# Performance work log

Hardware: AMD Instinct MI355X
Metric: run time of the kernel (lower is better)

The kernel has to match this reference:

```python
import jax, jax.numpy as jnp
import numpy as np

EPS = 1e-5
K = 20
LRELU = 0.2


def _bn(x, g, b, ch_axis):
    # inference BatchNorm with running_mean=0, running_var=1
    shape = [1] * x.ndim
    shape[ch_axis] = -1
    scale = (g / jnp.sqrt(1.0 + EPS)).reshape(shape)
    bias = b.reshape(shape)
    return x * scale + bias


def _lrelu(x):
    return jnp.where(x > 0, x, LRELU * x)


def _edge_conv(x, W, g, b):
    # x: (B, C, N) -> (B, C_out, N)
    B, C, N = x.shape
    xt = jnp.swapaxes(x, 1, 2)                      # (B, N, C)
    inner = -2.0 * jnp.einsum('bnc,bmc->bnm', xt, xt)
    xx = jnp.sum(xt * xt, axis=2)                   # (B, N)
    pdist = -xx[:, :, None] - inner - xx[:, None, :]  # negative sq dist (B,N,N)
    idx = jax.lax.top_k(pdist, K)[1]                # (B, N, K) nearest (incl. self)
    # gather neighbor features per batch: (C, N) indexed by (N, K) -> (C, N, K)
    neighbors = jax.vmap(lambda xf, id_: xf[:, id_])(x, idx)  # (B, C, N, K)
    center = jnp.broadcast_to(x[..., None], (B, C, N, K))
    edge = jnp.concatenate([center, neighbors - center], axis=1)  # (B, 2C, N, K)
    h = jnp.einsum('oc,bcnk->bonk', W, edge)        # 1x1 conv, no bias
    h = _lrelu(_bn(h, g, b, 1))
    return jnp.max(h, axis=-1)                      # (B, C_out, N)


def setup_inputs() -> dict:
    key = jax.random.key(0)
    ks = jax.random.split(key, 24)
    B, N = 4, 2048
    d = {}
    d['points'] = jax.random.normal(ks[0], (B, N, 3), dtype=jnp.float32)

    def w(k_, shape):
        return 0.1 * jax.random.normal(k_, shape, dtype=jnp.float32)

    def gam(k_, c):
        return 1.0 + 0.1 * jax.random.normal(k_, (c,), dtype=jnp.float32)

    def bet(k_, c):
        return 0.05 * jax.random.normal(k_, (c,), dtype=jnp.float32)

    # EdgeConv blocks: (out, 2*in)
    d['w1'], d['g1'], d['b1'] = w(ks[1], (64, 6)), gam(ks[2], 64), bet(ks[3], 64)
    d['w2'], d['g2'], d['b2'] = w(ks[4], (64, 128)), gam(ks[5], 64), bet(ks[6], 64)
    d['w3'], d['g3'], d['b3'] = w(ks[7], (128, 128)), gam(ks[8], 128), bet(ks[9], 128)
    d['w4'], d['g4'], d['b4'] = w(ks[10], (256, 256)), gam(ks[11], 256), bet(ks[12], 256)
    # conv5 1x1: 512 -> 1024
    d['w5'], d['g5'], d['b5'] = w(ks[13], (1024, 512)), gam(ks[14], 1024), bet(ks[15], 1024)
    # fc: 2048 -> 512 -> 256
    d['fw1'], d['fb1'] = w(ks[16], (512, 2048)), 0.05 * jax.random.normal(ks[17], (512,), dtype=jnp.float32)
    d['g6'], d['b6'] = gam(ks[18], 512), bet(ks[19], 512)
    d['fw2'], d['fb2'] = w(ks[20], (256, 512)), 0.05 * jax.random.normal(ks[21], (256,), dtype=jnp.float32)
    d['g7'], d['b7'] = gam(ks[22], 256), bet(ks[23], 256)
    return d


def reference(points, w1, g1, b1, w2, g2, b2, w3, g3, b3, w4, g4, b4,
              w5, g5, b5, fw1, fb1, g6, b6, fw2, fb2, g7, b7):
    x = jnp.swapaxes(points[:, :, :3], 1, 2)        # (B, 3, N)
    x1 = _edge_conv(x, w1, g1, b1)                  # (B, 64, N)
    x2 = _edge_conv(x1, w2, g2, b2)                 # (B, 64, N)
    x3 = _edge_conv(x2, w3, g3, b3)                 # (B, 128, N)
    x4 = _edge_conv(x3, w4, g4, b4)                 # (B, 256, N)
    h = jnp.concatenate([x1, x2, x3, x4], axis=1)   # (B, 512, N)
    h = _lrelu(_bn(jnp.einsum('oc,bcn->bon', w5, h), g5, b5, 1))  # (B, 1024, N)
    h_max = jnp.max(h, axis=-1)
    h_avg = jnp.mean(h, axis=-1)
    f = jnp.concatenate([h_max, h_avg], axis=1)     # (B, 2048)
    f = _lrelu(_bn(f @ fw1.T + fb1, g6, b6, 1))     # dropout = identity (eval)
    f = _bn(f @ fw2.T + fb2, g7, b7, 1)
    return f                                        # (B, 256)
```

## Files before the change

### kernel.cpp

```cpp
#include <hip/hip_runtime.h>
#include <hip/hip_bf16.h>
#include <float.h>

#define N_PTS 2048
#define B_SZ  4
#define KNN   20
#define LRELU_S 0.2f
#define FT    512
#define NPOOL 16

typedef __hip_bfloat16 bf16;
typedef __attribute__((ext_vector_type(8))) short short8v;
typedef __attribute__((ext_vector_type(4))) short short4v;
typedef __attribute__((ext_vector_type(4))) float floatx4;

__device__ __forceinline__ float b2f(const bf16 v) { return __bfloat162float(v); }
__device__ __forceinline__ float ldf(const float* p) { return *p; }
__device__ __forceinline__ float ldf(const bf16* p)  { return __bfloat162float(*p); }
__device__ __forceinline__ short8v ld8(const bf16* p) { return *(const short8v*)p; }
__device__ __forceinline__ unsigned umin(unsigned a, unsigned b) { return a < b ? a : b; }
__device__ __forceinline__ short bfbits(float f) {
    bf16 t = __float2bfloat16(f);
    return *reinterpret_cast<short*>(&t);
}

__device__ __forceinline__ void gload16(const void* g, void* l) {
    __builtin_amdgcn_global_load_lds(
        (const __attribute__((address_space(1))) void*)g,
        (__attribute__((address_space(3))) void*)l, 16, 0, 0);
}

__device__ __forceinline__ int sniff_body(const unsigned short* pts_hw) {
    int sane = 0;
    for (int j = 0; j < 64; ++j) {
        unsigned short v = pts_hw[2 * j];
        int e = (v >> 7) & 0xFF;
        if (e >= 100 && e <= 140) ++sane;
    }
    return (sane >= 32) ? 1 : 0;
}

__global__ void k_sniff(const unsigned short* __restrict__ pts_hw, int* __restrict__ flag) {
    if (threadIdx.x != 0 || blockIdx.x != 0) return;
    *flag = sniff_body(pts_hw);
}

struct WPack {
    const void* src[23];
    int off[24];
    int rows[23];
    int cols[23];
};

__device__ __forceinline__ void repack_body(const WPack& wp, int isb,
                                            float* __restrict__ dst, int i, int limit,
                                            int skip12) {
    if (i >= limit) return;
    int lo = 0, hi = 23;
    while (lo + 1 < hi) { int mid = (lo + hi) >> 1; if (i >= wp.off[mid]) lo = mid; else hi = mid; }
    if (skip12 && lo == 12) return;
    int j = i - wp.off[lo];
    float v = isb ? b2f(((const bf16*)wp.src[lo])[j]) : ((const float*)wp.src[lo])[j];
    int dj = j;
    int cols = wp.cols[lo];
    if (cols) dj = (j % cols) * wp.rows[lo] + (j / cols);
    dst[wp.off[lo] + dj] = v;
}

template<int C, int COUT>
__device__ __forceinline__ void wsplit_body(const void* __restrict__ W, int isb,
                                            bf16* __restrict__ dst, int i) {
    if (i >= COUT * C) return;
    int o = i / C, c = i % C;
    float w1 = isb ? b2f(((const bf16*)W)[(size_t)o * 2 * C + c])
                   : ((const float*)W)[(size_t)o * 2 * C + c];
    float w2 = isb ? b2f(((const bf16*)W)[(size_t)o * 2 * C + C + c])
                   : ((const float*)W)[(size_t)o * 2 * C + C + c];
    float wd = w1 - w2;
    bf16 h2 = __float2bfloat16(w2);
    bf16 hd = __float2bfloat16(wd);
    dst[i]                = h2;
    dst[COUT * C + i]     = __float2bfloat16(w2 - b2f(h2));
    dst[2 * COUT * C + i] = hd;
    dst[3 * COUT * C + i] = __float2bfloat16(wd - b2f(hd));
}

__device__ __forceinline__ void w5split_body(const void* __restrict__ W, int isb,
                                             bf16* __restrict__ dst, int i) {
    if (i >= 1024 * 512) return;
    float w = isb ? b2f(((const bf16*)W)[i]) : ((const float*)W)[i];
    bf16 h = __float2bfloat16(w);
    dst[i] = h;
    if (!isb) dst[1024 * 512 + i] = __float2bfloat16(w - b2f(h));
}

__device__ __forceinline__ void transpose_body(const void* __restrict__ pts, int isb,
                                               float* __restrict__ x0, int i) {
    if (i >= B_SZ * N_PTS) return;
    int b = i / N_PTS, n = i % N_PTS;
    for (int c = 0; c < 3; ++c) {
        size_t s = ((size_t)b * N_PTS + n) * 3 + c;
        float v = isb ? b2f(((const bf16*)pts)[s]) : ((const float*)pts)[s];
        x0[((size_t)b * 3 + c) * N_PTS + n] = v;
    }
}

__global__ void k_prep(WPack wp, float* __restrict__ wf, int rlimit,
                       const void* __restrict__ w2s, bf16* __restrict__ wsp2,
                       const void* __restrict__ w3s, bf16* __restrict__ wsp3,
                       const void* __restrict__ w4s, bf16* __restrict__ wsp4,
                       const void* __restrict__ w5s, bf16* __restrict__ w5sp,
                       const void* __restrict__ pts, float* __restrict__ x0,
                       int* __restrict__ flagout) {
    __shared__ int sfl;
    if (threadIdx.x == 0) {
        int f = sniff_body((const unsigned short*)pts);
        sfl = f;
        if (blockIdx.x == 0) *flagout = f;
    }
    __syncthreads();
    const int isb = sfl;
    const int nbrep = (rlimit + 255) >> 8;
    int ib = blockIdx.x, t = threadIdx.x;
    if (ib < nbrep) { repack_body(wp, isb, wf, ib * 256 + t, rlimit, 1); return; }
    ib -= nbrep;
    if (ib < 16)   { wsplit_body<64, 64>(w2s, isb, wsp2, ib * 256 + t); return; }
    ib -= 16;
    if (ib < 32)   { wsplit_body<64, 128>(w3s, isb, wsp3, ib * 256 + t); return; }
    ib -= 32;
    if (ib < 128)  { wsplit_body<128, 256>(w4s, isb, wsp4, ib * 256 + t); return; }
    ib -= 128;
    if (ib < 2048) { w5split_body(w5s, isb, w5sp, ib * 256 + t); return; }
    ib -= 2048;
    transpose_body(pts, isb, x0, ib * 256 + t);
}

__global__ void k_repack(WPack wp, const int* __restrict__ flag, float* __restrict__ dst, int limit) {
    repack_body(wp, *flag, dst, blockIdx.x * blockDim.x + threadIdx.x, limit, 0);
}
__global__ void k_transpose(const void* __restrict__ pts, const int* __restrict__ flag,
                            float* __restrict__ x0) {
    transpose_body(pts, *flag, x0, blockIdx.x * blockDim.x + threadIdx.x);
}

__device__ __forceinline__ void load32(const float* row, int mbase, float* r) {
    const float4* p = (const float4*)(row + mbase);
#pragma unroll
    for (int i = 0; i < 8; ++i) {
        float4 f = p[i];
        r[4 * i + 0] = f.x; r[4 * i + 1] = f.y; r[4 * i + 2] = f.z; r[4 * i + 3] = f.w;
    }
}
__device__ __forceinline__ void load32(const bf16* row, int mbase, float* r) {
    const uint4* p = (const uint4*)(row + mbase);
#pragma unroll
    for (int i = 0; i < 4; ++i) {
        uint4 u = p[i];
        r[8 * i + 0] = __uint_as_float(u.x << 16);
        r[8 * i + 1] = __uint_as_float(u.x & 0xFFFF0000u);
        r[8 * i + 2] = __uint_as_float(u.y << 16);
        r[8 * i + 3] = __uint_as_float(u.y & 0xFFFF0000u);
        r[8 * i + 4] = __uint_as_float(u.z << 16);
        r[8 * i + 5] = __uint_as_float(u.z & 0xFFFF0000u);
        r[8 * i + 6] = __uint_as_float(u.w << 16);
        r[8 * i + 7] = __uint_as_float(u.w & 0xFFFF0000u);
    }
}

__device__ __forceinline__ void s2ins(unsigned k, unsigned& m1, unsigned& m2) {
    unsigned lo = umin(m1, k);
    unsigned hi = (m1 < k) ? k : m1;
    m1 = lo;
    m2 = umin(m2, hi);
}

__device__ __forceinline__ void select20x2(const unsigned* ka, const unsigned* kb,
                                           int* outA, int* outB, int lane) {
    const unsigned SENT = 0xFFFFFFFFu;
    unsigned a1 = SENT, a2 = SENT, b1 = SENT, b2 = SENT;
#pragma unroll
    for (int j = 0; j < 32; ++j) {
        s2ins(ka[j], a1, a2);
        s2ins(kb[j], b1, b2);
    }
#pragma unroll 1
    for (int k = 0; k < KNN; ++k) {
        unsigned va = a1, vb = b1;
#pragma unroll
        for (int off = 32; off >= 1; off >>= 1) {
            va = umin(va, (unsigned)__shfl_xor((int)va, off));
            vb = umin(vb, (unsigned)__shfl_xor((int)vb, off));
        }
        if (lane == 0) { outA[k] = (int)(va & 2047u); outB[k] = (int)(vb & 2047u); }
        if (a1 == va) { a1 = a2; a2 = SENT; }
        if (b1 == vb) { b1 = b2; b2 = SENT; }
        if (a1 == SENT) {
#pragma unroll
            for (int j = 0; j < 32; ++j) {
                unsigned t = (ka[j] > va) ? ka[j] : SENT;
                s2ins(t, a1, a2);
            }
        }
        if (b1 == SENT) {
#pragma unroll
            for (int j = 0; j < 32; ++j) {
                unsigned t = (kb[j] > vb) ? kb[j] : SENT;
                s2ins(t, b1, b2);
            }
        }
    }
}

__global__ __launch_bounds__(256) void k_knn3ec(const float* __restrict__ x0,
        const float* __restrict__ Wt, const float* __restrict__ gam,
        const float* __restrict__ bet, bf16* __restrict__ featT,
        float* __restrict__ xxout) {
    __shared__ float qf[8][3];
    __shared__ int sidx[8][KNN];
    __shared__ float sh[8][KNN][3];
    int ib = blockIdx.x;
    int b  = ib / (N_PTS / 8);
    int q0 = (ib % (N_PTS / 8)) * 8;
    const float* xb = x0 + (size_t)b * 3 * N_PTS;

    if (threadIdx.x < 24) {
        int q = threadIdx.x / 3, c = threadIdx.x % 3;
        qf[q][c] = xb[(size_t)c * N_PTS + q0 + q];
    }
    __syncthreads();

    int w = threadIdx.x >> 6, lane = threadIdx.x & 63;
    int mbase = lane * 32;

    float da[32], db[32];
#pragma unroll
    for (int j = 0; j < 32; ++j) { da[j] = 0.f; db[j] = 0.f; }
#pragma unroll
    for (int c = 0; c < 3; ++c) {
        float r[32];
        load32(xb + (size_t)c * N_PTS, mbase, r);
        float qac = qf[2 * w][c], qbc = qf[2 * w + 1][c];
#pragma unroll
        for (int j = 0; j < 32; ++j) {
            float ta = r[j] - qac; da[j] = fmaf(ta, ta, da[j]);
            float tb = r[j] - qbc; db[j] = fmaf(tb, tb, db[j]);
        }
    }
    unsigned ka[32], kb[32];
#pragma unroll
    for (int j = 0; j < 32; ++j) {
        ka[j] = (__float_as_uint(da[j]) & 0xFFFFF800u) | (unsigned)(mbase + j);
        kb[j] = (__float_as_uint(db[j]) & 0xFFFFF800u) | (unsigned)(mbase + j);
    }
    select20x2(ka, kb, &sidx[2 * w][0], &sidx[2 * w + 1][0], lane);
    __syncthreads();

    for (int t = threadIdx.x; t < 8 * KNN * 3; t += 256) {
        int pt = t / (KNN * 3);
        int r  = t % (KNN * 3);
        int k = r / 3, c = r % 3;
        int m = sidx[pt][k] & (N_PTS - 1);
        sh[pt][k][c] = xb[(size_t)c * N_PTS + m];
    }
    __syncthreads();

    const float inv = rsqrtf(1.0f + 1e-5f);
    float scale = gam[lane] * inv, bias = bet[lane];
    float w1v[3], w2v[3];
#pragma unroll
    for (int c = 0; c < 3; ++c) {
        w1v[c] = Wt[(size_t)c * 64 + lane];
        w2v[c] = Wt[(size_t)(3 + c) * 64 + lane];
    }
#pragma unroll
    for (int p = 0; p < 2; ++p) {
        int pt = 2 * w + p;
        float base = 0.f;
#pragma unroll
        for (int c = 0; c < 3; ++c) base = fmaf(w1v[c] - w2v[c], qf[pt][c], base);
        float mx = -FLT_MAX;
#pragma unroll
        for (int k = 0; k < KNN; ++k) {
            float acc = 0.f;
#pragma unroll
            for (int c = 0; c < 3; ++c) acc = fmaf(w2v[c], sh[pt][k][c], acc);
            float h = (base + acc) * scale + bias;
            h = h > 0.f ? h : LRELU_S * h;
            mx = fmaxf(mx, h);
        }
        bf16 bv = __float2bfloat16(mx);
        size_t i = (size_t)b * N_PTS + q0 + pt;
        featT[i * FT + lane] = bv;
        float qv = b2f(bv);
        float s = qv * qv;
#pragma unroll
        for (int off = 32; off >= 1; off >>= 1) s += __shfl_xor(s, off);
        if (lane == 0) xxout[i] = s;
    }
}

template<typename T, int C>
__global__ __launch_bounds__(256) void k_knn(const T* __restrict__ x, int bstride,
                                             int* __restrict__ idx) {
    __shared__ float qf[4][C];
    int ib = blockIdx.x;
    int b  = ib / (N_PTS / 4);
    int q0 = (ib % (N_PTS / 4)) * 4;
    const T* xb = x + (size_t)b * bstride;

    for (int t = threadIdx.x; t < 4 * C; t += 256) {
        int pt = t / C, c = t % C;
        qf[pt][c] = ldf(&xb[(size_t)c * N_PTS + (q0 + pt)]);
    }
    __syncthreads();

    int w = threadIdx.x >> 6, lane = threadIdx.x & 63;
    int q = q0 + w;
    int mbase = lane * 32;

    float v[32];
#pragma unroll
    for (int j = 0; j < 32; ++j) v[j] = 0.f;

    for (int c = 0; c < C; ++c) {
        float qc = qf[w][c];
        float r[32];
        load32(xb + (size_t)c * N_PTS, mbase, r);
#pragma unroll
        for (int j = 0; j < 32; ++j) { float t = r[j] - qc; v[j] = fmaf(t, t, v[j]); }
    }

    for (int k = 0; k < KNN; ++k) {
        float bv = FLT_MAX; int bi = 0x7FFFFFFF;
#pragma unroll
        for (int j = 0; j < 32; ++j)
            if (v[j] < bv) { bv = v[j]; bi = mbase + j; }
#pragma unroll
        for (int off = 32; off >= 1; off >>= 1) {
            float ov = __shfl_xor(bv, off);
            int   oi = __shfl_xor(bi, off);
            if (ov < bv || (ov == bv && oi < bi)) { bv = ov; bi = oi; }
        }
        if (lane == 0) idx[((size_t)b * N_PTS + q) * KNN + k] = bi;
        int wl = bi >> 5, wj = bi & 31;
        if (lane == wl) {
#pragma unroll
            for (int j = 0; j < 32; ++j) if (j == wj) v[j] = FLT_MAX;
        }
    }
}

template<int C>
__device__ __forceinline__ void gram_body(const bf16* __restrict__ featT, int c0,
                                          float* __restrict__ G,
                                          short* At, short* Bt, int ib) {
    const int KC = 64;
    int b  = ib >> 8;
    int t  = ib & 255;
    int n0 = (t >> 4) << 7;
    int m0 = (t & 15) << 7;

    int tid = threadIdx.x;
    int w = tid >> 6, lane = tid & 63;
    int rw = (w & 1) * 64, cw = (w >> 1) * 64;
    int lrow = lane & 15, quad = lane >> 4;

    floatx4 acc[4][4];
#pragma unroll
    for (int ri = 0; ri < 4; ++ri)
#pragma unroll
        for (int ci = 0; ci < 4; ++ci) acc[ri][ci] = (floatx4){0.f, 0.f, 0.f, 0.f};

    for (int ck = 0; ck < C; ck += KC) {
        __syncthreads();
#pragma unroll
        for (int it = 0; it < 4; ++it) {
            int s = tid + it * 256;
            int row = s >> 3, seg = s & 7;
            int gseg = seg ^ (row & 7);
            gload16(featT + ((size_t)(b * N_PTS + n0 + row) * FT) + c0 + ck + gseg * 8,
                    &At[(s & ~63) * 8]);
            gload16(featT + ((size_t)(b * N_PTS + m0 + row) * FT) + c0 + ck + gseg * 8,
                    &Bt[(s & ~63) * 8]);
        }
        __syncthreads();
#pragma unroll
        for (int kk = 0; kk < KC; kk += 32) {
            int ks = kk >> 3;
            short8v a[4], bb[4];
#pragma unroll
            for (int ri = 0; ri < 4; ++ri) {
                int row = rw + ri * 16 + lrow;
                int seg = (ks + quad) ^ (row & 7);
                a[ri] = *(const short8v*)&At[row * 64 + seg * 8];
            }
#pragma unroll
            for (int ci = 0; ci < 4; ++ci) {
                int row = cw + ci * 16 + lrow;
                int seg = (ks + quad) ^ (row & 7);
                bb[ci] = *(const short8v*)&Bt[row * 64 + seg * 8];
            }
#pragma unroll
            for (int ri = 0; ri < 4; ++ri)
#pragma unroll
                for (int ci = 0; ci < 4; ++ci)
                    acc[ri][ci] = __builtin_amdgcn_mfma_f32_16x16x32_bf16(a[ri], bb[ci], acc[ri][ci], 0, 0, 0);
        }
    }

#pragma unroll
    for (int ri = 0; ri < 4; ++ri)
#pragma unroll
        for (int ci = 0; ci < 4; ++ci) {
            int n = n0 + rw + ri * 16 + quad * 4;
            int m = m0 + cw + ci * 16 + lrow;
            float* gp = G + ((size_t)b * N_PTS + n) * N_PTS + m;
#pragma unroll
            for (int reg = 0; reg < 4; ++reg)
                gp[(size_t)reg * N_PTS] = acc[ri][ci][reg];
        }
}

template<int COUT, int C>
__device__ __forceinline__ void xform_body(const bf16* __restrict__ featT, int c0,
                                           const bf16* __restrict__ Wsp,
                                           bf16* __restrict__ Yh, int isb,
                                           short* Bt, int ib2) {
    const int M2 = 2 * COUT;
    const int KC = 64;
    int nt = ib2 & 63;
    int mt = ib2 >> 6;
    int tid = threadIdx.x;
    int w = tid >> 6, lane = tid & 63;
    int rw = (w & 1) * 64, cw = (w >> 1) * 64;
    int l15 = lane & 15, quad = lane >> 4;

    floatx4 acc[4][4];
#pragma unroll
    for (int ri = 0; ri < 4; ++ri)
#pragma unroll
        for (int ci = 0; ci < 4; ++ci) acc[ri][ci] = (floatx4){0.f, 0.f, 0.f, 0.f};

    for (int ck = 0; ck < C; ck += KC) {
        __syncthreads();
#pragma unroll
        for (int it = 0; it < 4; ++it) {
            int s = tid + it * 256;
            int row = s >> 3, seg = s & 7;
            int gseg = seg ^ (row & 7);
            gload16(featT + (size_t)(nt * 128 + row) * FT + c0 + ck + gseg * 8,
                    &Bt[(s & ~63) * 8]);
        }
        __syncthreads();
#pragma unroll
        for (int kk = 0; kk < KC; kk += 32) {
            int ks = kk >> 3;
            short8v bfr[4];
#pragma unroll
            for (int ci = 0; ci < 4; ++ci) {
                int row = cw + ci * 16 + l15;
                int seg = (ks + quad) ^ (row & 7);
                bfr[ci] = *(const short8v*)&Bt[row * 64 + seg * 8];
            }
#pragma unroll
            for (int ri = 0; ri < 4; ++ri) {
                int rbase = mt * 128 + rw + ri * 16;
                bool uselo = (!isb) || (rbase >= COUT);
                int mrow = rbase + l15;
                int base = (mrow < COUT) ? mrow : (mrow + COUT);
                const bf16* hi = Wsp + (size_t)base * C + ck + kk + quad * 8;
                short8v ah = ld8(hi);
                short8v al;
                if (uselo) al = ld8(hi + (size_t)COUT * C);
#pragma unroll
                for (int ci = 0; ci < 4; ++ci) {
                    acc[ri][ci] = __builtin_amdgcn_mfma_f32_16x16x32_bf16(ah, bfr[ci], acc[ri][ci], 0, 0, 0);
                    if (uselo)
                        acc[ri][ci] = __builtin_amdgcn_mfma_f32_16x16x32_bf16(al, bfr[ci], acc[ri][ci], 0, 0, 0);
                }
            }
        }
    }

#pragma unroll
    for (int ri = 0; ri < 4; ++ri)
#pragma unroll
        for (int ci = 0; ci < 4; ++ci) {
            int n = nt * 128 + cw + ci * 16 + l15;
            int m = mt * 128 + rw + ri * 16 + quad * 4;
            short4v o4;
            o4[0] = bfbits(acc[ri][ci][0]);
            o4[1] = bfbits(acc[ri][ci][1]);
            o4[2] = bfbits(acc[ri][ci][2]);
            o4[3] = bfbits(acc[ri][ci][3]);
            *(short4v*)(Yh + (size_t)n * M2 + m) = o4;
        }
}

template<int C, int COUT>
__global__ __launch_bounds__(256) void k_gx(const bf16* __restrict__ featT, int c0,
        const bf16* __restrict__ Wsp, float* __restrict__ G, bf16* __restrict__ Yh,
        const int* __restrict__ flag) {
    __shared__ __align__(16) short lds[2 * 128 * 64];
    int ib = blockIdx.x;
    if (ib < B_SZ * 256) {
        gram_body<C>(featT, c0, G, lds, lds + 128 * 64, ib);
    } else {
        xform_body<COUT, C>(featT, c0, Wsp, Yh, *flag, lds, ib - B_SZ * 256);
    }
}

template<int COUT>
__global__ __launch_bounds__(256) void k_selgmax(const float* __restrict__ G,
        const float* __restrict__ xxin, const bf16* __restrict__ Yh,
        const float* __restrict__ gam, const float* __restrict__ bet,
        bf16* __restrict__ featT, int c0f, float* __restrict__ xxout) {
    const int M2 = 2 * COUT;
    const int OT = COUT / 64;
    __shared__ int sidx[8][KNN];

    int ib = blockIdx.x;
    int b  = ib / (N_PTS / 8);
    int q0 = (ib % (N_PTS / 8)) * 8;
    int w = threadIdx.x >> 6, lane = threadIdx.x & 63;
    int qa = q0 + 2 * w;
    const float* gA = G + ((size_t)b * N_PTS + qa) * N_PTS;
    const float* gB = gA + N_PTS;
    const float* xr = xxin + (size_t)b * N_PTS;
    float xqa = xr[qa], xqb = xr[qa + 1];

    unsigned ka[32], kb[32];
#pragma unroll
    for (int r = 0; r < 8; ++r) {
        int m0 = r * 256 + (lane << 2);
        float4 x4 = *(const float4*)(xr + m0);
        float4 a4 = *(const float4*)(gA + m0);
        float4 b4 = *(const float4*)(gB + m0);
        float s;
        s = fmaf(-2.f, a4.x, x4.x) + xqa; s = fmaxf(s, 0.f);
        ka[4 * r + 0] = (__float_as_uint(s) & 0xFFFFF800u) | (unsigned)(m0 + 0);
        s = fmaf(-2.f, a4.y, x4.y) + xqa; s = fmaxf(s, 0.f);
        ka[4 * r + 1] = (__float_as_uint(s) & 0xFFFFF800u) | (unsigned)(m0 + 1);
        s = fmaf(-2.f, a4.z, x4.z) + xqa; s = fmaxf(s, 0.f);
        ka[4 * r + 2] = (__float_as_uint(s) & 0xFFFFF800u) | (unsigned)(m0 + 2);
        s = fmaf(-2.f, a4.w, x4.w) + xqa; s = fmaxf(s, 0.f);
        ka[4 * r + 3] = (__float_as_uint(s) & 0xFFFFF800u) | (unsigned)(m0 + 3);
        s = fmaf(-2.f, b4.x, x4.x) + xqb; s = fmaxf(s, 0.f);
        kb[4 * r + 0] = (__float_as_uint(s) & 0xFFFFF800u) | (unsigned)(m0 + 0);
        s = fmaf(-2.f, b4.y, x4.y) + xqb; s = fmaxf(s, 0.f);
        kb[4 * r + 1] = (__float_as_uint(s) & 0xFFFFF800u) | (unsigned)(m0 + 1);
        s = fmaf(-2.f, b4.z, x4.z) + xqb; s = fmaxf(s, 0.f);
        kb[4 * r + 2] = (__float_as_uint(s) & 0xFFFFF800u) | (unsigned)(m0 + 2);
        s = fmaf(-2.f, b4.w, x4.w) + xqb; s = fmaxf(s, 0.f);
        kb[4 * r + 3] = (__float_as_uint(s) & 0xFFFFF800u) | (unsigned)(m0 + 3);
    }
    select20x2(ka, kb, &sidx[2 * w][0], &sidx[2 * w + 1][0], lane);
    __syncthreads();

    size_t iA = (size_t)b * N_PTS + qa;
    const float inv = rsqrtf(1.0f + 1e-5f);
    float yda[OT], ydb[OT], scl[OT], bis[OT], mxa[OT], mxb[OT];
#pragma unroll
    for (int j = 0; j < OT; ++j) {
        int o = lane + 64 * j;
        yda[j] = b2f(Yh[iA * M2 + COUT + o]);
        ydb[j] = b2f(Yh[(iA + 1) * M2 + COUT + o]);
        scl[j] = gam[o] * inv;
        bis[j] = bet[o];
        mxa[j] = -FLT_MAX; mxb[j] = -FLT_MAX;
    }
    const bf16* Yb = Yh + (size_t)b * N_PTS * M2;
#pragma unroll
    for (int k = 0; k < KNN; ++k) {
        int m0 = sidx[2 * w][k] & (N_PTS - 1);
        int m1 = sidx[2 * w + 1][k] & (N_PTS - 1);
        const bf16* r0 = Yb + (size_t)m0 * M2;
        const bf16* r1 = Yb + (size_t)m1 * M2;
#pragma unroll
        for (int j = 0; j < OT; ++j) {
            int o = lane + 64 * j;
            float ha = (yda[j] + b2f(r0[o])) * scl[j] + bis[j];
            ha = ha > 0.f ? ha : LRELU_S * ha;
            mxa[j] = fmaxf(mxa[j], ha);
            float hb = (ydb[j] + b2f(r1[o])) * scl[j] + bis[j];
            hb = hb > 0.f ? hb : LRELU_S * hb;
            mxb[j] = fmaxf(mxb[j], hb);
        }
    }
    float sa = 0.f, sb = 0.f;
#pragma unroll
    for (int j = 0; j < OT; ++j) {
        bf16 va = __float2bfloat16(mxa[j]);
        bf16 vb = __float2bfloat16(mxb[j]);
        featT[iA * FT + c0f + lane + 64 * j] = va;
        featT[(iA + 1) * FT + c0f + lane + 64 * j] = vb;
        if (xxout) {
            float pa = b2f(va); sa = fmaf(pa, pa, sa);
            float pb = b2f(vb); sb = fmaf(pb, pb, sb);
        }
    }
    if (xxout) {
#pragma unroll
        for (int off = 32; off >= 1; off >>= 1) {
            sa += __shfl_xor(sa, off);
            sb += __shfl_xor(sb, off);
        }
        if (lane == 0) { xxout[iA] = sa; xxout[iA + 1] = sb; }
    }
}

template<typename T, int C, int COUT, bool WF>
__global__ __launch_bounds__(256) void k_edgeconv(const T* __restrict__ x, int bstride,
                           const int* __restrict__ idx,
                           const float* __restrict__ Wt,
                           const float* __restrict__ gam,
                           const float* __restrict__ bet,
                           bf16* __restrict__ out, int ostride,
                           bf16* __restrict__ featT, int c0f,
                           float* __restrict__ xxout) {
    const int PT = 4;
    const int OT = COUT / 64;
    const int CP = (C + 3) & ~3;
    __shared__ float sh[PT][KNN + 1][CP];

    int ib = blockIdx.x;
    int b  = ib / (N_PTS / PT);
    int n0 = (ib % (N_PTS / PT)) * PT;
    const T* xb = x + (size_t)b * bstride;

    const int TOT = PT * (KNN + 1) * C;
    for (int t = threadIdx.x; t < TOT; t += 256) {
        int pt = t / ((KNN + 1) * C);
        int r  = t % ((KNN + 1) * C);
        int row = r / C, c = r % C;
        int n = n0 + pt;
        int m = (row == 0) ? n
                           : (idx[((size_t)b * N_PTS + n) * KNN + (row - 1)] & (N_PTS - 1));
        sh[pt][row][c] = ldf(&xb[(size_t)c * N_PTS + m]);
    }
    __syncthreads();

    int w = threadIdx.x >> 6, lane = threadIdx.x & 63;
    int n = n0 + w;

    constexpr int KT = (OT >= 4) ? 10 : 20;
    constexpr int NPASS = KNN / KT;

    float base[OT];
    float mx[OT];
#pragma unroll
    for (int j = 0; j < OT; ++j) { base[j] = 0.f; mx[j] = -FLT_MAX; }

    const float inv = rsqrtf(1.0f + 1e-5f);

#pragma unroll
    for (int pass = 0; pass < NPASS; ++pass) {
        float acc[OT][KT];
#pragma unroll
        for (int j = 0; j < OT; ++j)
#pragma unroll
            for (int k = 0; k < KT; ++k) acc[j][k] = 0.f;

        for (int c = 0; c < C; ++c) {
            float xq = sh[w][0][c];
            float w2v[OT];
#pragma unroll
            for (int j = 0; j < OT; ++j)
                w2v[j] = Wt[(size_t)(C + c) * COUT + lane + 64 * j];
            if (pass == 0) {
#pragma unroll
                for (int j = 0; j < OT; ++j) {
                    float w1v = Wt[(size_t)c * COUT + lane + 64 * j];
                    base[j] = fmaf(w1v - w2v[j], xq, base[j]);
                }
            }
#pragma unroll
            for (int k = 0; k < KT; ++k) {
                float nv = sh[w][1 + pass * KT + k][c];
#pragma unroll
                for (int j = 0; j < OT; ++j) acc[j][k] = fmaf(w2v[j], nv, acc[j][k]);
            }
        }

#pragma unroll
        for (int j = 0; j < OT; ++j) {
            int o = lane + 64 * j;
            float scale = gam[o] * inv, bias = bet[o];
#pragma unroll
            for (int k = 0; k < KT; ++k) {
                float h = (base[j] + acc[j][k]) * scale + bias;
                h = h > 0.f ? h : LRELU_S * h;
                mx[j] = fmaxf(mx[j], h);
            }
        }
    }

    float s = 0.f;
#pragma unroll
    for (int j = 0; j < OT; ++j) {
        int o = lane + 64 * j;
        bf16 bv = __float2bfloat16(mx[j]);
        if (!WF) out[(size_t)b * ostride + (size_t)o * N_PTS + n] = bv;
        if (WF) {
            featT[((size_t)b * N_PTS + n) * FT + c0f + o] = bv;
            float q = b2f(bv);
            s = fmaf(q, q, s);
        }
    }
    if (WF && xxout) {
#pragma unroll
        for (int off = 32; off >= 1; off >>= 1) s += __shfl_xor(s, off);
        if (lane == 0) xxout[(size_t)b * N_PTS + n] = s;
    }
}

__global__ __launch_bounds__(256) void k_conv5mfma(
        const bf16* __restrict__ featT, const bf16* __restrict__ w5sp,
        const float* __restrict__ g5, const float* __restrict__ b5,
        float* __restrict__ fmxp, float* __restrict__ fsmp,
        const int* __restrict__ flag) {
    __shared__ __align__(16) short Bt[128 * 64];
    __shared__ __align__(16) short Ah[64 * 64];
    __shared__ __align__(16) short Al[64 * 64];
    __shared__ float rmx[4][64];
    __shared__ float rsm[4][64];

    const int isb = *flag;
    int ib = blockIdx.x;
    int b  = ib / 256;
    int rem = ib % 256;
    int o0 = (rem >> 4) * 64;
    int nt = rem & 15;
    int tid = threadIdx.x;
    int w = tid >> 6, lane = tid & 63;
    int l15 = lane & 15, quad = lane >> 4;

    const bf16* Whi = w5sp;
    const bf16* Wlo = w5sp + 1024 * 512;
    const bf16* fb  = featT + (size_t)b * N_PTS * FT;
    const int nbase0 = nt * 128;

    floatx4 acc[4][2];
#pragma unroll
    for (int mi = 0; mi < 4; ++mi)
#pragma unroll
        for (int ni = 0; ni < 2; ++ni) acc[mi][ni] = (floatx4){0.f, 0.f, 0.f, 0.f};

    for (int ck = 0; ck < 512; ck += 64) {
        __syncthreads();
#pragma unroll
        for (int it = 0; it < 4; ++it) {
            int s = tid + it * 256;
            int row = s >> 3, seg = s & 7;
            int gseg = seg ^ (row & 7);
            gload16(fb + (size_t)(nbase0 + row) * FT + ck + gseg * 8,
                    &Bt[(s & ~63) * 8]);
        }
#pragma unroll
        for (int it = 0; it < 2; ++it) {
            int s = tid + it * 256;
            int row = s >> 3, seg = s & 7;
            int gseg = seg ^ (row & 7);
            gload16(Whi + (size_t)(o0 + row) * 512 + ck + gseg * 8, &Ah[(s & ~63) * 8]);
            if (!isb)
                gload16(Wlo + (size_t)(o0 + row) * 512 + ck + gseg * 8, &Al[(s & ~63) * 8]);
        }
        __syncthreads();
#pragma unroll
        for (int kk = 0; kk < 64; kk += 32) {
            int ks = kk >> 3;
            short8v bfr[2], ah[4], al[4];
#pragma unroll
            for (int ni = 0; ni < 2; ++ni) {
                int row = w * 32 + ni * 16 + l15;
                int seg = (ks + quad) ^ (row & 7);
                bfr[ni] = *(const short8v*)&Bt[row * 64 + seg * 8];
            }
#pragma unroll
            for (int mi = 0; mi < 4; ++mi) {
                int row = mi * 16 + l15;
                int seg = (ks + quad) ^ (row & 7);
                ah[mi] = *(const short8v*)&Ah[row * 64 + seg * 8];
                if (!isb) al[mi] = *(const short8v*)&Al[row * 64 + seg * 8];
            }
#pragma unroll
            for (int mi = 0; mi < 4; ++mi)
#pragma unroll
                for (int ni = 0; ni < 2; ++ni) {
                    acc[mi][ni] = __builtin_amdgcn_mfma_f32_16x16x32_bf16(ah[mi], bfr[ni], acc[mi][ni], 0, 0, 0);
                    if (!isb)
                        acc[mi][ni] = __builtin_amdgcn_mfma_f32_16x16x32_bf16(al[mi], bfr[ni], acc[mi][ni], 0, 0, 0);
                }
        }
    }

    const float inv = rsqrtf(1.0f + 1e-5f);
#pragma unroll
    for (int mi = 0; mi < 4; ++mi) {
#pragma unroll
        for (int r = 0; r < 4; ++r) {
            int o = o0 + mi * 16 + quad * 4 + r;
            float scale = g5[o] * inv, bias = b5[o];
            float mx = -FLT_MAX, sm = 0.f;
#pragma unroll
            for (int ni = 0; ni < 2; ++ni) {
                float h = acc[mi][ni][r] * scale + bias;
                h = h > 0.f ? h : LRELU_S * h;
                mx = fmaxf(mx, h);
                sm += h;
            }
#pragma unroll
            for (int off = 1; off <= 8; off <<= 1) {
                mx = fmaxf(mx, __shfl_xor(mx, off));
                sm += __shfl_xor(sm, off);
            }
            if (l15 == 0) {
                rmx[w][mi * 16 + quad * 4 + r] = mx;
                rsm[w][mi * 16 + quad * 4 + r] = sm;
            }
        }
    }
    __syncthreads();
    if (tid < 64) {
        float mx = -FLT_MAX, sm = 0.f;
#pragma unroll
        for (int ww = 0; ww < 4; ++ww) { mx = fmaxf(mx, rmx[ww][tid]); sm += rsm[ww][tid]; }
        fmxp[((size_t)b * 1024 + o0 + tid) * NPOOL + nt] = mx;
        fsmp[((size_t)b * 1024 + o0 + tid) * NPOOL + nt] = sm;
    }
}

__global__ void k_pool(const float* __restrict__ fmxp, const float* __restrict__ fsmp,
                       float* __restrict__ fvec) {
    int i = blockIdx.x * blockDim.x + threadIdx.x;
    if (i >= B_SZ * 1024) return;
    int b = i >> 10, o = i & 1023;
    float mx = -FLT_MAX, sm = 0.f;
    for (int ch = 0; ch < NPOOL; ++ch) {
        mx = fmaxf(mx, fmxp[(size_t)i * NPOOL + ch]);
        sm += fsmp[(size_t)i * NPOOL + ch];
    }
    fvec[(size_t)b * 2048 + o] = mx;
    fvec[(size_t)b * 2048 + 1024 + o] = sm * (1.0f / N_PTS);
}

__global__ __launch_bounds__(256) void k_fc1(const float* __restrict__ fvec,
        const void* __restrict__ fw1, const void* __restrict__ fb1,
        const void* __restrict__ g6,  const void* __restrict__ b6,
        const int* __restrict__ flag, float* __restrict__ tbuf) {
    __shared__ float red[4];
    int ib = blockIdx.x;
    int b = ib >> 9, o = ib & 511;
    const float* fv = fvec + (size_t)b * 2048;
    int tid = threadIdx.x;
    const int isb = *flag;
    float s = 0.f;
    if (isb) {
        const bf16* wr = (const bf16*)fw1 + (size_t)o * 2048;
        for (int j = tid; j < 2048; j += 256) s = fmaf(b2f(wr[j]), fv[j], s);
    } else {
        const float* wr = (const float*)fw1 + (size_t)o * 2048;
        for (int j = tid; j < 2048; j += 256) s = fmaf(wr[j], fv[j], s);
    }
#pragma unroll
    for (int off = 32; off >= 1; off >>= 1) s += __shfl_xor(s, off);
    if ((tid & 63) == 0) red[tid >> 6] = s;
    __syncthreads();
    if (tid == 0) {
        float fb = isb ? b2f(((const bf16*)fb1)[o]) : ((const float*)fb1)[o];
        float gg = isb ? b2f(((const bf16*)g6)[o])  : ((const float*)g6)[o];
        float bb = isb ? b2f(((const bf16*)b6)[o])  : ((const float*)b6)[o];
        float acc = fb + red[0] + red[1] + red[2] + red[3];
        float h = acc * gg * rsqrtf(1.0f + 1e-5f) + bb;
        tbuf[(size_t)b * 512 + o] = h > 0.f ? h : LRELU_S * h;
    }
}

__global__ __launch_bounds__(256) void k_fc2(const float* __restrict__ tbuf,
        const void* __restrict__ fw2, const void* __restrict__ fb2,
        const void* __restrict__ g7,  const void* __restrict__ b7,
        const int* __restrict__ flag, void* __restrict__ out) {
    __shared__ float red[4];
    int ib = blockIdx.x;
    int b = ib >> 8, o = ib & 255;
    const float* tv = tbuf + (size_t)b * 512;
    int tid = threadIdx.x;
    const int isb = *flag;
    float s;
    if (isb) {
        const bf16* wr = (const bf16*)fw2 + (size_t)o * 512;
        s = fmaf(b2f(wr[tid]), tv[tid], b2f(wr[tid + 256]) * tv[tid + 256]);
    } else {
        const float* wr = (const float*)fw2 + (size_t)o * 512;
        s = fmaf(wr[tid], tv[tid], wr[tid + 256] * tv[tid + 256]);
    }
#pragma unroll
    for (int off = 32; off >= 1; off >>= 1) s += __shfl_xor(s, off);
    if ((tid & 63) == 0) red[tid >> 6] = s;
    __syncthreads();
    if (tid == 0) {
        float fb = isb ? b2f(((const bf16*)fb2)[o]) : ((const float*)fb2)[o];
        float gg = isb ? b2f(((const bf16*)g7)[o])  : ((const float*)g7)[o];
        float bb = isb ? b2f(((const bf16*)b7)[o])  : ((const float*)b7)[o];
        float acc = fb + red[0] + red[1] + red[2] + red[3];
        float h = acc * gg * rsqrtf(1.0f + 1e-5f) + bb;
        if (isb) ((bf16*)out)[(size_t)b * 256 + o] = __float2bfloat16(h);
        else     ((float*)out)[(size_t)b * 256 + o] = h;
    }
}

#define NCH 2
__global__ __launch_bounds__(256) void k_conv5pool(const bf16* __restrict__ feat,
                            const float* __restrict__ w5,
                            const float* __restrict__ g5,
                            const float* __restrict__ b5,
                            float* __restrict__ fmxp, float* __restrict__ fsmp) {
    const int OT = 8;
    const int NT = 4;
    const int CHN = N_PTS / NCH;
    __shared__ float wl[OT][512];
    __shared__ float rmx[4][OT];
    __shared__ float rsm[4][OT];

    int ib = blockIdx.x;
    int ch = ib % NCH;
    int ot = (ib / NCH) % (1024 / OT);
    int b  = ib / (NCH * (1024 / OT));
    int o0 = ot * OT;
    const bf16* fb = feat + (size_t)b * 512 * N_PTS;

    for (int t = threadIdx.x; t < OT * 512; t += 256) {
        int o = t >> 9, c = t & 511;
        wl[o][c] = w5[(size_t)(o0 + o) * 512 + c];
    }
    __syncthreads();

    const int n0 = ch * CHN + threadIdx.x * NT;

    float acc[OT][NT];
#pragma unroll
    for (int o = 0; o < OT; ++o)
#pragma unroll
        for (int t = 0; t < NT; ++t) acc[o][t] = 0.f;

    for (int c = 0; c < 512; c += 4) {
        float fv[4][NT];
#pragma unroll
        for (int j = 0; j < 4; ++j) {
            uint2 u = *(const uint2*)(fb + (size_t)(c + j) * N_PTS + n0);
            fv[j][0] = __uint_as_float(u.x << 16);
            fv[j][1] = __uint_as_float(u.x & 0xFFFF0000u);
            fv[j][2] = __uint_as_float(u.y << 16);
            fv[j][3] = __uint_as_float(u.y & 0xFFFF0000u);
        }
#pragma unroll
        for (int o = 0; o < OT; ++o) {
            float4 wv = *(const float4*)&wl[o][c];
#pragma unroll
            for (int t = 0; t < NT; ++t) {
                acc[o][t] = fmaf(wv.x, fv[0][t], acc[o][t]);
                acc[o][t] = fmaf(wv.y, fv[1][t], acc[o][t]);
                acc[o][t] = fmaf(wv.z, fv[2][t], acc[o][t]);
                acc[o][t] = fmaf(wv.w, fv[3][t], acc[o][t]);
            }
        }
    }

    const float inv = rsqrtf(1.0f + 1e-5f);
    int w = threadIdx.x >> 6, lane = threadIdx.x & 63;
#pragma unroll
    for (int o = 0; o < OT; ++o) {
        float scale = g5[o0 + o] * inv, bias = b5[o0 + o];
        float mx = -FLT_MAX, sm = 0.f;
#pragma unroll
        for (int t = 0; t < NT; ++t) {
            float h = acc[o][t] * scale + bias;
            h = h > 0.f ? h : LRELU_S * h;
            mx = fmaxf(mx, h);
            sm += h;
        }
#pragma unroll
        for (int off = 32; off >= 1; off >>= 1) {
            mx = fmaxf(mx, __shfl_xor(mx, off));
            sm += __shfl_xor(sm, off);
        }
        if (lane == 0) { rmx[w][o] = mx; rsm[w][o] = sm; }
    }
    __syncthreads();
    if (threadIdx.x < OT) {
        int o = threadIdx.x;
        float mx = -FLT_MAX, sm = 0.f;
#pragma unroll
        for (int ww = 0; ww < 4; ++ww) { mx = fmaxf(mx, rmx[ww][o]); sm += rsm[ww][o]; }
        fmxp[((size_t)b * 1024 + o0 + o) * NCH + ch] = mx;
        fsmp[((size_t)b * 1024 + o0 + o) * NCH + ch] = sm;
    }
}

__global__ void k_head(const float* __restrict__ fmxp, const float* __restrict__ fsmp,
                       const float* __restrict__ fw1, const float* __restrict__ fb1,
                       const float* __restrict__ g6,  const float* __restrict__ b6,
                       const float* __restrict__ fw2, const float* __restrict__ fb2,
                       const float* __restrict__ g7,  const float* __restrict__ b7,
                       const int* __restrict__ flag, void* __restrict__ out) {
    __shared__ float f[2048];
    __shared__ float t[512];
    int b = blockIdx.x;
    for (int i = threadIdx.x; i < 1024; i += 256) {
        float mx = -FLT_MAX, sm = 0.f;
        for (int ch = 0; ch < NCH; ++ch) {
            mx = fmaxf(mx, fmxp[((size_t)b * 1024 + i) * NCH + ch]);
            sm += fsmp[((size_t)b * 1024 + i) * NCH + ch];
        }
        f[i]        = mx;
        f[1024 + i] = sm * (1.0f / N_PTS);
    }
    __syncthreads();
    const float inv = rsqrtf(1.0f + 1e-5f);
    for (int o = threadIdx.x; o < 512; o += 256) {
        const float* wr = fw1 + (size_t)o * 2048;
        float acc = fb1[o];
        for (int j = 0; j < 2048; ++j) acc += wr[j] * f[j];
        float h = acc * g6[o] * inv + b6[o];
        t[o] = h > 0.f ? h : LRELU_S * h;
    }
    __syncthreads();
    {
        int o = threadIdx.x;
        const float* wr = fw2 + (size_t)o * 512;
        float acc = fb2[o];
        for (int j = 0; j < 512; ++j) acc += wr[j] * t[j];
        float h = acc * g7[o] * inv + b7[o];
        if (*flag) ((bf16*)out)[(size_t)b * 256 + o] = __float2bfloat16(h);
        else       ((float*)out)[(size_t)b * 256 + o] = h;
    }
}

extern "C" void kernel_launch(void* const* d_in, const int* in_sizes, int n_in,
                              void* d_out, int out_size, void* d_ws, size_t ws_size,
                              hipStream_t stream) {
    static const int wsz[23] = {
        384, 64, 64,   8192, 64, 64,   16384, 128, 128,   65536, 256, 256,
        524288, 1024, 1024,   1048576, 512,   512, 512,   131072, 256,   256, 256
    };
    static const int trows[23] = {64,0,0, 64,0,0, 128,0,0, 256,0,0, 0,0,0, 0,0, 0,0, 0,0, 0,0};
    static const int tcols[23] = { 6,0,0,128,0,0, 128,0,0, 256,0,0, 0,0,0, 0,0, 0,0, 0,0, 0,0};

    WPack wp;
    int total = 0;
    for (int i = 0; i < 23; ++i) {
        wp.src[i] = d_in[i + 1]; wp.off[i] = total; total += wsz[i];
        wp.rows[i] = trows[i]; wp.cols[i] = tcols[i];
    }
    wp.off[23] = total;

    const size_t flag_bytes = 16;
    const size_t x0_bytes   = (size_t)B_SZ * 3 * N_PTS * 4;
    const size_t feat_bytes = (size_t)B_SZ * 512 * N_PTS * 2;
    const size_t idx_bytes  = (size_t)B_SZ * N_PTS * KNN * 4;
    const size_t pool_bytes = (size_t)B_SZ * 1024 * 4 * 2;
    const size_t wf_bytes   = (size_t)total * 4;
    const size_t base_need  = flag_bytes + x0_bytes + feat_bytes + idx_bytes + pool_bytes + wf_bytes;

    const size_t featT_bytes = (size_t)B_SZ * N_PTS * FT * 2;
    const size_t xx_bytes    = (size_t)B_SZ * N_PTS * 4;
    const size_t wsp2_elems  = 4 * 64 * 64;
    const size_t wsp3_elems  = 4 * 128 * 64;
    const size_t wsp4_elems  = 4 * 256 * 128;
    const size_t w5sp_elems  = 2 * 1024 * 512;
    const size_t wsp_bytes   = (wsp2_elems + wsp3_elems + wsp4_elems + w5sp_elems) * 2;
    const size_t Yh_bytes    = (size_t)B_SZ * N_PTS * 512 * 2;
    const size_t S_bytes     = (size_t)B_SZ * N_PTS * N_PTS * 4;
    const size_t full_need   = base_need + featT_bytes + 2 * xx_bytes + wsp_bytes
                             + Yh_bytes + S_bytes;

    if (ws_size < base_need) return;
    const bool use_gram = (ws_size >= full_need);

    char* w = (char*)d_ws;
    int*   flag = (int*)w;              w += flag_bytes;
    float* x0   = (float*)w;            w += x0_bytes;
    bf16*  feat = (bf16*)w;             w += feat_bytes;
    int*   idx  = (int*)w;              w += idx_bytes;
    w += pool_bytes;
    float* wf   = (float*)w;            w += wf_bytes;
    bf16*  featT = (bf16*)w;            w += featT_bytes;
    float* xxA   = (float*)w;           w += xx_bytes;
    float* xxB   = (float*)w;           w += xx_bytes;
    bf16*  wsp2  = (bf16*)w;            w += wsp2_elems * 2;
    bf16*  wsp3  = (bf16*)w;            w += wsp3_elems * 2;
    bf16*  wsp4  = (bf16*)w;            w += wsp4_elems * 2;
    bf16*  w5sp  = (bf16*)w;            w += w5sp_elems * 2;
    bf16*  Yh    = (bf16*)w;            w += Yh_bytes;
    float* S     = (float*)w;

    float* fmxp = (float*)idx;
    float* fsmp = fmxp + (size_t)B_SZ * 1024 * NPOOL;
    float* fvec = fsmp + (size_t)B_SZ * 1024 * NPOOL;
    float* tbuf = fvec + (size_t)B_SZ * 2048;

    const int FBS = 512 * N_PTS;

    const float* w1t = wf + wp.off[0],  *g1 = wf + wp.off[1],  *b1 = wf + wp.off[2];
    const float* w2t = wf + wp.off[3],  *g2 = wf + wp.off[4],  *b2 = wf + wp.off[5];
    const float* w3t = wf + wp.off[6],  *g3 = wf + wp.off[7],  *b3 = wf + wp.off[8];
    const float* w4t = wf + wp.off[9],  *g4 = wf + wp.off[10], *b4 = wf + wp.off[11];
    const float* w5  = wf + wp.off[12], *g5 = wf + wp.off[13], *b5 = wf + wp.off[14];
    const float* fw1 = wf + wp.off[15], *fb1 = wf + wp.off[16];
    const float* g6  = wf + wp.off[17], *b6 = wf + wp.off[18];
    const float* fw2 = wf + wp.off[19], *fb2 = wf + wp.off[20];
    const float* g7  = wf + wp.off[21], *b7 = wf + wp.off[22];

    const int GK = B_SZ * N_PTS / 4;
    const int G8 = B_SZ * N_PTS / 8;
    const int NG = B_SZ * 256;

    if (use_gram) {
        const int rlimit = wp.off[15];
        const int nbrep = (rlimit + 255) / 256;
        const int prep_grid = nbrep + 16 + 32 + 128 + 2048 + 32;
        k_prep<<<prep_grid, 256, 0, stream>>>(wp, wf, rlimit,
                                              d_in[4], wsp2, d_in[7], wsp3,
                                              d_in[10], wsp4, d_in[13], w5sp,
                                              d_in[0], x0, flag);

        k_knn3ec<<<G8, 256, 0, stream>>>(x0, w1t, g1, b1, featT, xxA);
        k_gx<64, 64><<<NG + 64, 256, 0, stream>>>(featT, 0, wsp2, S, Yh, flag);
        k_selgmax<64><<<G8, 256, 0, stream>>>(S, xxA, Yh, g2, b2, featT, 64, xxB);
        k_gx<64, 128><<<NG + 128, 256, 0, stream>>>(featT, 64, wsp3, S, Yh, flag);
        k_selgmax<128><<<G8, 256, 0, stream>>>(S, xxB, Yh, g3, b3, featT, 128, xxA);
        k_gx<128, 256><<<NG + 256, 256, 0, stream>>>(featT, 128, wsp4, S, Yh, flag);
        k_selgmax<256><<<G8, 256, 0, stream>>>(S, xxA, Yh, g4, b4, featT, 256, nullptr);

        k_conv5mfma<<<B_SZ * 256, 256, 0, stream>>>(featT, w5sp, g5, b5, fmxp, fsmp, flag);
        k_pool<<<(B_SZ * 1024 + 255) / 256, 256, 0, stream>>>(fmxp, fsmp, fvec);
        k_fc1<<<B_SZ * 512, 256, 0, stream>>>(fvec, d_in[16], d_in[17], d_in[18], d_in[19],
                                              flag, tbuf);
        k_fc2<<<B_SZ * 256, 256, 0, stream>>>(tbuf, d_in[20], d_in[21], d_in[22], d_in[23],
                                              flag, d_out);
    } else {
        k_sniff<<<1, 64, 0, stream>>>((const unsigned short*)d_in[0], flag);
        k_repack<<<(total + 255) / 256, 256, 0, stream>>>(wp, flag, wf, total);
        k_transpose<<<(B_SZ * N_PTS + 255) / 256, 256, 0, stream>>>(d_in[0], flag, x0);

        k_knn<float, 3><<<GK, 256, 0, stream>>>(x0, 3 * N_PTS, idx);
        k_edgeconv<float, 3, 64, false><<<GK, 256, 0, stream>>>(
            x0, 3 * N_PTS, idx, w1t, g1, b1, feat + 0 * N_PTS, FBS, nullptr, 0, nullptr);
        k_knn<bf16, 64><<<GK, 256, 0, stream>>>(feat + 0 * N_PTS, FBS, idx);
        k_edgeconv<bf16, 64, 64, false><<<GK, 256, 0, stream>>>(
            feat + 0 * N_PTS, FBS, idx, w2t, g2, b2, feat + 64 * N_PTS, FBS, nullptr, 0, nullptr);
        k_knn<bf16, 64><<<GK, 256, 0, stream>>>(feat + 64 * N_PTS, FBS, idx);
        k_edgeconv<bf16, 64, 128, false><<<GK, 256, 0, stream>>>(
            feat + 64 * N_PTS, FBS, idx, w3t, g3, b3, feat + 128 * N_PTS, FBS, nullptr, 0, nullptr);
        k_knn<bf16, 128><<<GK, 256, 0, stream>>>(feat + 128 * N_PTS, FBS, idx);
        k_edgeconv<bf16, 128, 256, false><<<GK, 256, 0, stream>>>(
            feat + 128 * N_PTS, FBS, idx, w4t, g4, b4, feat + 256 * N_PTS, FBS, nullptr, 0, nullptr);

        k_conv5pool<<<B_SZ * (1024 / 8) * NCH, 256, 0, stream>>>(feat, w5, g5, b5, fmxp, fsmp);
        k_head<<<B_SZ, 256, 0, stream>>>(fmxp, fsmp, fw1, fb1, g6, b6, fw2, fb2, g7, b7,
                                         flag, d_out);
    }
}
```

Baseline: 351.6 us.

## Fuse distance epilogue into Gram GEMM and store distances as fp16

The Gram kernel now computes the squared distance (xx_n + xx_m - 2*dot, clamped at zero) in its epilogue and stores it as fp16 instead of the raw fp32 dot product. The selection kernel reads the halved-size matrix with 16-byte vector loads and only decodes to float to build its sort keys. This halves write and read traffic on the large N×N intermediate and removes the xx loads from the selection kernel. The cost is reduced precision in the distances, which can change neighbor choice on near ties or overflow for large feature norms. The stores are also 2-byte scattered writes, which may coalesce less well.

```diff
diff --git a/kernel.cpp b/kernel.cpp
--- a/kernel.cpp
+++ b/kernel.cpp
@@ -22,6 +22,15 @@
 __device__ __forceinline__ short bfbits(float f) {
     bf16 t = __float2bfloat16(f);
     return *reinterpret_cast<short*>(&t);
+}
+__device__ __forceinline__ unsigned short f2h(float f) {
+    _Float16 h = (_Float16)f;
+    return *reinterpret_cast<unsigned short*>(&h);
+}
+__device__ __forceinline__ float h2f(unsigned short u) {
+    _Float16 h;
+    *reinterpret_cast<unsigned short*>(&h) = u;
+    return (float)h;
 }
 
 __device__ __forceinline__ void gload16(const void* g, void* l) {
@@ -352,7 +361,8 @@
 
 template<int C>
 __device__ __forceinline__ void gram_body(const bf16* __restrict__ featT, int c0,
-                                          float* __restrict__ G,
+                                          const float* __restrict__ xx,
+                                          unsigned short* __restrict__ D,
                                           short* At, short* Bt, int ib) {
     const int KC = 64;
     int b  = ib >> 8;
@@ -408,16 +418,31 @@
         }
     }
 
+    const float* xr = xx + (size_t)b * N_PTS;
+    float xmv[4];
+#pragma unroll
+    for (int ci = 0; ci < 4; ++ci)
+        xmv[ci] = xr[m0 + cw + ci * 16 + lrow];
+    float xnv[4][4];
+#pragma unroll
+    for (int ri = 0; ri < 4; ++ri)
+#pragma unroll
+        for (int reg = 0; reg < 4; ++reg)
+            xnv[ri][reg] = xr[n0 + rw + ri * 16 + quad * 4 + reg];
+
 #pragma unroll
     for (int ri = 0; ri < 4; ++ri)
 #pragma unroll
         for (int ci = 0; ci < 4; ++ci) {
             int n = n0 + rw + ri * 16 + quad * 4;
             int m = m0 + cw + ci * 16 + lrow;
-            float* gp = G + ((size_t)b * N_PTS + n) * N_PTS + m;
-#pragma unroll
-            for (int reg = 0; reg < 4; ++reg)
-                gp[(size_t)reg * N_PTS] = acc[ri][ci][reg];
+            unsigned short* gp = D + ((size_t)b * N_PTS + n) * N_PTS + m;
+#pragma unroll
+            for (int reg = 0; reg < 4; ++reg) {
+                float d = fmaf(-2.f, acc[ri][ci][reg], xmv[ci]) + xnv[ri][reg];
+                d = fmaxf(d, 0.f);
+                gp[(size_t)reg * N_PTS] = f2h(d);
+            }
         }
 }
 
@@ -499,20 +524,21 @@
 
 template<int C, int COUT>
 __global__ __launch_bounds__(256) void k_gx(const bf16* __restrict__ featT, int c0,
-        const bf16* __restrict__ Wsp, float* __restrict__ G, bf16* __restrict__ Yh,
+        const bf16* __restrict__ Wsp, const float* __restrict__ xx,
+        unsigned short* __restrict__ D, bf16* __restrict__ Yh,
         const int* __restrict__ flag) {
     __shared__ __align__(16) short lds[2 * 128 * 64];
     int ib = blockIdx.x;
     if (ib < B_SZ * 256) {
-        gram_body<C>(featT, c0, G, lds, lds + 128 * 64, ib);
+        gram_body<C>(featT, c0, xx, D, lds, lds + 128 * 64, ib);
     } else {
         xform_body<COUT, C>(featT, c0, Wsp, Yh, *flag, lds, ib - B_SZ * 256);
     }
 }
 
 template<int COUT>
-__global__ __launch_bounds__(256) void k_selgmax(const float* __restrict__ G,
-        const float* __restrict__ xxin, const bf16* __restrict__ Yh,
+__global__ __launch_bounds__(256) void k_selgmax(const unsigned short* __restrict__ D,
+        const bf16* __restrict__ Yh,
         const float* __restrict__ gam, const float* __restrict__ bet,
         bf16* __restrict__ featT, int c0f, float* __restrict__ xxout) {
     const int M2 = 2 * COUT;
@@ -524,35 +550,28 @@
     int q0 = (ib % (N_PTS / 8)) * 8;
     int w = threadIdx.x >> 6, lane = threadIdx.x & 63;
     int qa = q0 + 2 * w;
-    const float* gA = G + ((size_t)b * N_PTS + qa) * N_PTS;
-    const float* gB = gA + N_PTS;
-    const float* xr = xxin + (size_t)b * N_PTS;
-    float xqa = xr[qa], xqb = xr[qa + 1];
+    const unsigned short* gA = D + ((size_t)b * N_PTS + qa) * N_PTS;
+    const unsigned short* gB = gA + N_PTS;
 
     unsigned ka[32], kb[32];
 #pragma unroll
-    for (int r = 0; r < 8; ++r) {
-        int m0 = r * 256 + (lane << 2);
-        float4 x4 = *(const float4*)(xr + m0);
-        float4 a4 = *(const float4*)(gA + m0);
-        float4 b4 = *(const float4*)(gB + m0);
-        float s;
-        s = fmaf(-2.f, a4.x, x4.x) + xqa; s = fmaxf(s, 0.f);
-        ka[4 * r + 0] = (__float_as_uint(s) & 0xFFFFF800u) | (unsigned)(m0 + 0);
-        s = fmaf(-2.f, a4.y, x4.y) + xqa; s = fmaxf(s, 0.f);
-        ka[4 * r + 1] = (__float_as_uint(s) & 0xFFFFF800u) | (unsigned)(m0 + 1);
-        s = fmaf(-2.f, a4.z, x4.z) + xqa; s = fmaxf(s, 0.f);
-        ka[4 * r + 2] = (__float_as_uint(s) & 0xFFFFF800u) | (unsigned)(m0 + 2);
-        s = fmaf(-2.f, a4.w, x4.w) + xqa; s = fmaxf(s, 0.f);
-        ka[4 * r + 3] = (__float_as_uint(s) & 0xFFFFF800u) | (unsigned)(m0 + 3);
-        s = fmaf(-2.f, b4.x, x4.x) + xqb; s = fmaxf(s, 0.f);
-        kb[4 * r + 0] = (__float_as_uint(s) & 0xFFFFF800u) | (unsigned)(m0 + 0);
-        s = fmaf(-2.f, b4.y, x4.y) + xqb; s = fmaxf(s, 0.f);
-        kb[4 * r + 1] = (__float_as_uint(s) & 0xFFFFF800u) | (unsigned)(m0 + 1);
-        s = fmaf(-2.f, b4.z, x4.z) + xqb; s = fmaxf(s, 0.f);
-        kb[4 * r + 2] = (__float_as_uint(s) & 0xFFFFF800u) | (unsigned)(m0 + 2);
-        s = fmaf(-2.f, b4.w, x4.w) + xqb; s = fmaxf(s, 0.f);
-        kb[4 * r + 3] = (__float_as_uint(s) & 0xFFFFF800u) | (unsigned)(m0 + 3);
+    for (int r = 0; r < 4; ++r) {
+        int m0 = r * 512 + (lane << 3);
+        uint4 ua = *(const uint4*)(gA + m0);
+        uint4 ub = *(const uint4*)(gB + m0);
+        unsigned uw[4] = {ua.x, ua.y, ua.z, ua.w};
+        unsigned vw[4] = {ub.x, ub.y, ub.z, ub.w};
+#pragma unroll
+        for (int h = 0; h < 4; ++h) {
+            float a0 = h2f((unsigned short)(uw[h] & 0xFFFFu));
+            float a1 = h2f((unsigned short)(uw[h] >> 16));
+            ka[8 * r + 2 * h]     = (__float_as_uint(a0) & 0xFFFFF800u) | (unsigned)(m0 + 2 * h);
+            ka[8 * r + 2 * h + 1] = (__float_as_uint(a1) & 0xFFFFF800u) | (unsigned)(m0 + 2 * h + 1);
+            float c0v = h2f((unsigned short)(vw[h] & 0xFFFFu));
+            float c1v = h2f((unsigned short)(vw[h] >> 16));
+            kb[8 * r + 2 * h]     = (__float_as_uint(c0v) & 0xFFFFF800u) | (unsigned)(m0 + 2 * h);
+            kb[8 * r + 2 * h + 1] = (__float_as_uint(c1v) & 0xFFFFF800u) | (unsigned)(m0 + 2 * h + 1);
+        }
     }
     select20x2(ka, kb, &sidx[2 * w][0], &sidx[2 * w + 1][0], lane);
     __syncthreads();
@@ -1070,7 +1089,7 @@
     const size_t w5sp_elems  = 2 * 1024 * 512;
     const size_t wsp_bytes   = (wsp2_elems + wsp3_elems + wsp4_elems + w5sp_elems) * 2;
     const size_t Yh_bytes    = (size_t)B_SZ * N_PTS * 512 * 2;
-    const size_t S_bytes     = (size_t)B_SZ * N_PTS * N_PTS * 4;
+    const size_t S_bytes     = (size_t)B_SZ * N_PTS * N_PTS * 2;
     const size_t full_need   = base_need + featT_bytes + 2 * xx_bytes + wsp_bytes
                              + Yh_bytes + S_bytes;
 
@@ -1092,7 +1111,7 @@
     bf16*  wsp4  = (bf16*)w;            w += wsp4_elems * 2;
     bf16*  w5sp  = (bf16*)w;            w += w5sp_elems * 2;
     bf16*  Yh    = (bf16*)w;            w += Yh_bytes;
-    float* S     = (float*)w;
+    unsigned short* D = (unsigned short*)w;
 
     float* fmxp = (float*)idx;
     float* fsmp = fmxp + (size_t)B_SZ * 1024 * NPOOL;
@@ -1125,12 +1144,12 @@
                                               d_in[0], x0, flag);
 
         k_knn3ec<<<G8, 256, 0, stream>>>(x0, w1t, g1, b1, featT, xxA);
-        k_gx<64, 64><<<NG + 64, 256, 0, stream>>>(featT, 0, wsp2, S, Yh, flag);
-        k_selgmax<64><<<G8, 256, 0, stream>>>(S, xxA, Yh, g2, b2, featT, 64, xxB);
-        k_gx<64, 128><<<NG + 128, 256, 0, stream>>>(featT, 64, wsp3, S, Yh, flag);
-        k_selgmax<128><<<G8, 256, 0, stream>>>(S, xxB, Yh, g3, b3, featT, 128, xxA);
-        k_gx<128, 256><<<NG + 256, 256, 0, stream>>>(featT, 128, wsp4, S, Yh, flag);
-        k_selgmax<256><<<G8, 256, 0, stream>>>(S, xxA, Yh, g4, b4, featT, 256, nullptr);
+        k_gx<64, 64><<<NG + 64, 256, 0, stream>>>(featT, 0, wsp2, xxA, D, Yh, flag);
+        k_selgmax<64><<<G8, 256, 0, stream>>>(D, Yh, g2, b2, featT, 64, xxB);
+        k_gx<64, 128><<<NG + 128, 256, 0, stream>>>(featT, 64, wsp3, xxB, D, Yh, flag);
+        k_selgmax<128><<<G8, 256, 0, stream>>>(D, Yh, g3, b3, featT, 128, xxA);
+        k_gx<128, 256><<<NG + 256, 256, 0, stream>>>(featT, 128, wsp4, xxA, D, Yh, flag);
+        k_selgmax<256><<<G8, 256, 0, stream>>>(D, Yh, g4, b4, featT, 256, nullptr);
 
         k_conv5mfma<<<B_SZ * 256, 256, 0, stream>>>(featT, w5sp, g5, b5, fmxp, fsmp, flag);
         k_pool<<<(B_SZ * 1024 + 255) / 256, 256, 0, stream>>>(fmxp, fsmp, fvec);
```

After: 332.3 us. 5.5% less time.
